# Kernel tuning notes

Hardware: AMD Instinct MI355X
Metric: run time of the kernel (lower is better)

The kernel has to match this reference:

```python
import jax, jax.numpy as jnp
import numpy as np

N = 20000
E = 400000
LATENT = 128
HIDDEN = 512
OUT = 64
HEADS = 4
NEG_SLOPE = 0.2


def setup_inputs() -> dict:
    key = jax.random.key(0)
    ks = jax.random.split(key, 12)
    z = jax.random.normal(ks[0], (N, LATENT), dtype=jnp.float32)
    edge_index = jax.random.randint(ks[1], (2, E), 0, N, dtype=jnp.int64)
    h1 = HIDDEN // 2
    # dense1, dense2 (torch Linear: y = x @ W.T + b; store W already transposed)
    W1 = jax.random.normal(ks[2], (LATENT, h1), dtype=jnp.float32) / np.sqrt(LATENT)
    b1 = jnp.zeros((h1,), dtype=jnp.float32)
    W2 = jax.random.normal(ks[3], (h1, HIDDEN), dtype=jnp.float32) / np.sqrt(h1)
    b2 = jnp.zeros((HIDDEN,), dtype=jnp.float32)
    # GATConv params
    Wg = jax.random.normal(ks[4], (HIDDEN, HEADS * OUT), dtype=jnp.float32) / np.sqrt(HIDDEN)
    att_src = jax.random.normal(ks[5], (HEADS, OUT), dtype=jnp.float32) * 0.1
    att_dst = jax.random.normal(ks[6], (HEADS, OUT), dtype=jnp.float32) * 0.1
    bias_g = jnp.zeros((OUT,), dtype=jnp.float32)
    return {"z": z, "W1": W1, "b1": b1, "W2": W2, "b2": b2,
            "Wg": Wg, "att_src": att_src, "att_dst": att_dst, "bias_g": bias_g,
            "edge_index": edge_index}


def _gat(x, Wg, att_src, att_dst, bias_g, src, dst):
    # project: [N, H, D]
    h = (x @ Wg).reshape(N, HEADS, OUT)
    a_src = jnp.einsum('nhd,hd->nh', h, att_src)  # [N, H]
    a_dst = jnp.einsum('nhd,hd->nh', h, att_dst)
    e = a_src[src] + a_dst[dst]                   # [E+N, H]
    e = jax.nn.leaky_relu(e, NEG_SLOPE)
    # segment softmax over destination nodes
    m = jax.ops.segment_max(e, dst, num_segments=N)
    e = jnp.exp(e - m[dst])
    denom = jax.ops.segment_sum(e, dst, num_segments=N)
    w = e / (denom[dst] + 1e-16)                  # [E+N, H]
    msg = h[src] * w[:, :, None]                  # [E+N, H, D]
    out = jax.ops.segment_sum(msg, dst, num_segments=N)  # [N, H, D]
    return out.mean(axis=1) + bias_g              # concat=False -> mean heads


def reference(z, W1, b1, W2, b2, Wg, att_src, att_dst, bias_g, edge_index):
    x = jax.nn.relu(z @ W1 + b1)
    x = jax.nn.relu(x @ W2 + b2)
    # PyG GATConv default add_self_loops=True
    loop = jnp.arange(N, dtype=edge_index.dtype)
    src = jnp.concatenate([edge_index[0], loop])
    dst = jnp.concatenate([edge_index[1], loop])
    return _gat(x, Wg, att_src, att_dst, bias_g, src, dst)
```

## Files before the change

### kernel.cpp

```cpp
#include <hip/hip_runtime.h>
#include <hip/hip_bf16.h>

#define N_NODES 20000
#define MPAD    20096
#define E_EDGES 400000
#define LATENT 128
#define H1 256
#define HIDDEN 512
#define OUT_D 64
#define HEADS 4
#define NEG_SLOPE 0.2f
#define MAX_IN 80

typedef __attribute__((ext_vector_type(8))) __bf16 bf16x8;
typedef __attribute__((ext_vector_type(4))) float f32x4;
typedef __attribute__((ext_vector_type(4))) unsigned short u16x4;
typedef __attribute__((ext_vector_type(8))) unsigned short u16x8;

__device__ __forceinline__ unsigned short f2bf(float f) {
    union { float f; unsigned int u; } v; v.f = f;
    unsigned int r = v.u + 0x7fffu + ((v.u >> 16) & 1u);
    return (unsigned short)(r >> 16);
}
__device__ __forceinline__ float bf2f(unsigned short u) {
    union { unsigned int u; float f; } v; v.u = ((unsigned int)u) << 16;
    return v.f;
}

#define W1_TILES 32
#define W2_TILES 128
#define WG_TILES 128
#define CUR_BLKS ((N_NODES + 255) / 256)
#define PREP_BLKS (W1_TILES + W2_TILES + WG_TILES + CUR_BLKS)
__global__ __launch_bounds__(256)
void prep_kernel(const float* __restrict__ W1, const float* __restrict__ W2,
                 const float* __restrict__ Wg,
                 unsigned short* __restrict__ W1t, unsigned short* __restrict__ W2t,
                 unsigned short* __restrict__ Wgt, int* __restrict__ cur) {
    int b = blockIdx.x;
    if (b >= W1_TILES + W2_TILES + WG_TILES) {
        int t = (b - (W1_TILES + W2_TILES + WG_TILES)) * 256 + threadIdx.x;
        if (t < N_NODES) cur[t] = 0;
        return;
    }
    const float* src; unsigned short* dst; int K, N, k0, n0;
    if (b < W1_TILES) {
        src = W1; dst = W1t; K = LATENT; N = H1;
        k0 = (b >> 3) * 32; n0 = (b & 7) * 32;
    } else if (b < W1_TILES + W2_TILES) {
        int t2 = b - W1_TILES;
        src = W2; dst = W2t; K = H1; N = HIDDEN;
        k0 = (t2 >> 4) * 32; n0 = (t2 & 15) * 32;
    } else {
        int t3 = b - W1_TILES - W2_TILES;
        src = Wg; dst = Wgt; K = HIDDEN; N = HEADS * OUT_D;
        k0 = (t3 >> 3) * 32; n0 = (t3 & 7) * 32;
    }
    __shared__ float tile[32][33];
    const int c = threadIdx.x & 31, r0 = threadIdx.x >> 5;
#pragma unroll
    for (int i = 0; i < 4; i++) {
        int r = r0 + i * 8;
        tile[r][c] = src[(size_t)(k0 + r) * N + n0 + c];
    }
    __syncthreads();
#pragma unroll
    for (int i = 0; i < 4; i++) {
        int r = r0 + i * 8;
        dst[(size_t)(n0 + r) * K + k0 + c] = f2bf(tile[c][r]);
    }
}

#define TM 32
#define ZPITCH 136
#define XPITCH 264
#define X2PITCH 520
#define MLP_BLOCKS (MPAD / TM)
#define SCAT_BLOCKS ((E_EDGES + 255) / 256)
__global__ __launch_bounds__(256, 4)
void mlp_scatter_kernel(const float* __restrict__ z,
                        const unsigned short* __restrict__ W1t,
                        const unsigned short* __restrict__ W2t,
                        const unsigned short* __restrict__ Wgt,
                        const float* __restrict__ b1, const float* __restrict__ b2,
                        const float* __restrict__ att_src, const float* __restrict__ att_dst,
                        const int* __restrict__ ei, int* __restrict__ cur,
                        int* __restrict__ adj,
                        unsigned short* __restrict__ hb,
                        float* __restrict__ a_src, float* __restrict__ a_dst) {
    __shared__ unsigned short x2s[TM * X2PITCH];
    __shared__ unsigned short x1s[TM * XPITCH];

    if (blockIdx.x >= MLP_BLOCKS) {
        int t = (blockIdx.x - MLP_BLOCKS) * 256 + threadIdx.x;
        if (t < E_EDGES) {
            int s = ei[t], d = ei[E_EDGES + t];
            int idx = atomicAdd(&cur[d], 1);
            idx = min(idx, MAX_IN - 1);
            adj[d * MAX_IN + idx] = s;
        }
        return;
    }

    unsigned short* zbf = x2s;
    const int tid = threadIdx.x;
    const int wave = tid >> 6, lane = tid & 63;
    const int m0 = blockIdx.x * TM;
    const int fr = lane & 15, q = lane >> 4;

#define LDW1(kt, t)      (*(const bf16x8*)(W1t + (size_t)(nb1 + (t) * 16 + fr) * LATENT + (kt) * 32 + q * 8))
#define LDW2H(nh, kt, t) (*(const bf16x8*)(W2t + (size_t)(nb2 + (nh) * 64 + (t) * 16 + fr) * H1 + (kt) * 32 + q * 8))
#define LDW3(kt, t)      (*(const bf16x8*)(Wgt + (size_t)(nb3 + (t) * 16 + fr) * HIDDEN + (kt) * 32 + q * 8))

    const int nb1 = wave * 64;
    const int nb2 = wave * 128;
    const int head = wave;
    const int nb3 = wave * 64;

    bf16x8 w1a[4], w1b[4];
#pragma unroll
    for (int t = 0; t < 4; t++) w1a[t] = LDW1(0, t);

    {
        const int r = tid >> 3, c0 = (tid & 7) * 16;
        const int zrow = min(m0 + r, N_NODES - 1);
        const float* zp = z + (size_t)zrow * LATENT + c0;
#pragma unroll
        for (int i = 0; i < 4; i++) {
            f32x4 v = *(const f32x4*)(zp + i * 4);
            u16x4 p = { f2bf(v[0]), f2bf(v[1]), f2bf(v[2]), f2bf(v[3]) };
            *(u16x4*)(zbf + r * ZPITCH + c0 + i * 4) = p;
        }
    }
    __syncthreads();

    f32x4 acc1[2][4] = {};
#pragma unroll
    for (int kt = 0; kt < 4; kt++) {
        bf16x8* wc = (kt & 1) ? w1b : w1a;
        bf16x8* wn = (kt & 1) ? w1a : w1b;
        if (kt < 3) {
#pragma unroll
            for (int t = 0; t < 4; t++) wn[t] = LDW1(kt + 1, t);
        }
        bf16x8 af[2];
#pragma unroll
        for (int t = 0; t < 2; t++)
            af[t] = *(const bf16x8*)(zbf + (t * 16 + fr) * ZPITCH + kt * 32 + q * 8);
#pragma unroll
        for (int mt = 0; mt < 2; mt++)
#pragma unroll
            for (int nt = 0; nt < 4; nt++)
                acc1[mt][nt] = __builtin_amdgcn_mfma_f32_16x16x32_bf16(
                    wc[nt], af[mt], acc1[mt][nt], 0, 0, 0);
    }

    bf16x8 w2a[4], w2b[4];
#pragma unroll
    for (int t = 0; t < 4; t++) w2a[t] = LDW2H(0, 0, t);

#pragma unroll
    for (int nt = 0; nt < 4; nt++) {
        const int n = nb1 + nt * 16 + q * 4;
        const f32x4 bv = *(const f32x4*)(b1 + n);
#pragma unroll
        for (int mt = 0; mt < 2; mt++) {
            u16x4 p;
#pragma unroll
            for (int r = 0; r < 4; r++) p[r] = f2bf(fmaxf(acc1[mt][nt][r] + bv[r], 0.f));
            *(u16x4*)(x1s + (mt * 16 + fr) * XPITCH + n) = p;
        }
    }
    __syncthreads();

#pragma unroll
    for (int nh = 0; nh < 2; nh++) {
        if (nh == 1) {
#pragma unroll
            for (int t = 0; t < 4; t++) w2a[t] = LDW2H(1, 0, t);
        }
        f32x4 acc2[2][4] = {};
#pragma unroll
        for (int kt = 0; kt < 8; kt++) {
            bf16x8* wc = (kt & 1) ? w2b : w2a;
            bf16x8* wn = (kt & 1) ? w2a : w2b;
            if (kt < 7) {
#pragma unroll
                for (int t = 0; t < 4; t++) wn[t] = LDW2H(nh, kt + 1, t);
            }
            bf16x8 af[2];
#pragma unroll
            for (int t = 0; t < 2; t++)
                af[t] = *(const bf16x8*)(x1s + (t * 16 + fr) * XPITCH + kt * 32 + q * 8);
#pragma unroll
            for (int mt = 0; mt < 2; mt++)
#pragma unroll
                for (int nt = 0; nt < 4; nt++)
                    acc2[mt][nt] = __builtin_amdgcn_mfma_f32_16x16x32_bf16(
                        wc[nt], af[mt], acc2[mt][nt], 0, 0, 0);
        }
#pragma unroll
        for (int nt = 0; nt < 4; nt++) {
            const int n = nb2 + nh * 64 + nt * 16 + q * 4;
            const f32x4 bv = *(const f32x4*)(b2 + n);
#pragma unroll
            for (int mt = 0; mt < 2; mt++) {
                u16x4 p;
#pragma unroll
                for (int r = 0; r < 4; r++) p[r] = f2bf(fmaxf(acc2[mt][nt][r] + bv[r], 0.f));
                *(u16x4*)(x2s + (mt * 16 + fr) * X2PITCH + n) = p;
            }
        }
    }

    bf16x8 w3a[4], w3b[4];
#pragma unroll
    for (int t = 0; t < 4; t++) w3a[t] = LDW3(0, t);
    __syncthreads();

    f32x4 acc3[2][4] = {};
#pragma unroll
    for (int kt = 0; kt < 16; kt++) {
        bf16x8* wc = (kt & 1) ? w3b : w3a;
        bf16x8* wn = (kt & 1) ? w3a : w3b;
        if (kt < 15) {
#pragma unroll
            for (int t = 0; t < 4; t++) wn[t] = LDW3(kt + 1, t);
        }
        bf16x8 af[2];
#pragma unroll
        for (int t = 0; t < 2; t++)
            af[t] = *(const bf16x8*)(x2s + (t * 16 + fr) * X2PITCH + kt * 32 + q * 8);
#pragma unroll
        for (int mt = 0; mt < 2; mt++)
#pragma unroll
            for (int nt = 0; nt < 4; nt++)
                acc3[mt][nt] = __builtin_amdgcn_mfma_f32_16x16x32_bf16(
                    wc[nt], af[mt], acc3[mt][nt], 0, 0, 0);
    }

    {
        f32x4 asv[4], adv[4];
#pragma unroll
        for (int nt = 0; nt < 4; nt++) {
            asv[nt] = *(const f32x4*)(att_src + head * OUT_D + nt * 16 + q * 4);
            adv[nt] = *(const f32x4*)(att_dst + head * OUT_D + nt * 16 + q * 4);
        }
#pragma unroll
        for (int mt = 0; mt < 2; mt++) {
            const int row = m0 + mt * 16 + fr;
            float vs = 0.f, vd = 0.f;
#pragma unroll
            for (int nt = 0; nt < 4; nt++) {
                u16x4 p;
#pragma unroll
                for (int r = 0; r < 4; r++) {
                    float x = acc3[mt][nt][r];
                    p[r] = f2bf(x);
                    vs += x * asv[nt][r];
                    vd += x * adv[nt][r];
                }
                *(u16x4*)(hb + (size_t)row * (HEADS * OUT_D) + head * OUT_D + nt * 16 + q * 4) = p;
            }
            vs += __shfl_xor(vs, 16, 64); vs += __shfl_xor(vs, 32, 64);
            vd += __shfl_xor(vd, 16, 64); vd += __shfl_xor(vd, 32, 64);
            if (q == 0 && row < N_NODES) {
                a_src[row * HEADS + head] = vs;
                a_dst[row * HEADS + head] = vd;
            }
        }
    }
#undef LDW1
#undef LDW2H
#undef LDW3
}

__global__ __launch_bounds__(256)
void fused_gat(const int* __restrict__ adj, const int* __restrict__ cur,
               const float* __restrict__ a_src, const float* __restrict__ a_dst,
               const unsigned short* __restrict__ hb,
               const float* __restrict__ bias_g, float* __restrict__ out) {
    const int wave = threadIdx.x >> 6, lane = threadIdx.x & 63;
    const int grp = lane >> 5, sl = lane & 31;
    const int d = blockIdx.x * 8 + wave * 2 + grp;
    const int h = sl >> 3, j = sl & 7;
    const int cnt = min(cur[d], MAX_IN);
    const int* arow = adj + d * MAX_IN;
    const int gbase = grp * 32;

    int myadj = (sl < cnt) ? arow[sl] : 0;

    const float ad = a_dst[d * HEADS + h];
    const unsigned short* hp = hb + h * OUT_D + j * 8;

    float vself = a_src[d * HEADS + h] + ad;
    vself = (vself > 0.f) ? vself : NEG_SLOPE * vself;
    float sm = __expf(fminf(vself, 60.f));
    u16x8 gs = *(const u16x8*)(hp + (size_t)d * (HEADS * OUT_D));
    float acc[8];
#pragma unroll
    for (int r = 0; r < 8; r++) acc[r] = sm * bf2f(gs[r]);

    const int lim = cnt < 32 ? cnt : 32;
    int e = 0;
    for (; e + 7 < lim; e += 8) {
        int sx[8]; float fx[8]; u16x8 gx[8];
#pragma unroll
        for (int u = 0; u < 8; u++) sx[u] = __shfl(myadj, gbase + e + u, 64);
#pragma unroll
        for (int u = 0; u < 8; u++) fx[u] = a_src[sx[u] * HEADS + h];
#pragma unroll
        for (int u = 0; u < 8; u++) gx[u] = *(const u16x8*)(hp + (size_t)sx[u] * (HEADS * OUT_D));
#pragma unroll
        for (int u = 0; u < 8; u++) {
            float v = fx[u] + ad;
            v = (v > 0.f) ? v : NEG_SLOPE * v;
            float w = __expf(fminf(v, 60.f));
            sm += w;
#pragma unroll
            for (int r = 0; r < 8; r++) acc[r] += w * bf2f(gx[u][r]);
        }
    }
    for (; e + 3 < lim; e += 4) {
        int sx[4]; float fx[4]; u16x8 gx[4];
#pragma unroll
        for (int u = 0; u < 4; u++) sx[u] = __shfl(myadj, gbase + e + u, 64);
#pragma unroll
        for (int u = 0; u < 4; u++) fx[u] = a_src[sx[u] * HEADS + h];
#pragma unroll
        for (int u = 0; u < 4; u++) gx[u] = *(const u16x8*)(hp + (size_t)sx[u] * (HEADS * OUT_D));
#pragma unroll
        for (int u = 0; u < 4; u++) {
            float v = fx[u] + ad;
            v = (v > 0.f) ? v : NEG_SLOPE * v;
            float w = __expf(fminf(v, 60.f));
            sm += w;
#pragma unroll
            for (int r = 0; r < 8; r++) acc[r] += w * bf2f(gx[u][r]);
        }
    }
    for (; e < lim; e++) {
        int s = __shfl(myadj, gbase + e, 64);
        float v = a_src[s * HEADS + h] + ad;
        v = (v > 0.f) ? v : NEG_SLOPE * v;
        float w = __expf(fminf(v, 60.f));
        u16x8 g = *(const u16x8*)(hp + (size_t)s * (HEADS * OUT_D));
        sm += w;
#pragma unroll
        for (int r = 0; r < 8; r++) acc[r] += w * bf2f(g[r]);
    }
    for (int e2 = 32; e2 < cnt; e2++) {
        int s = arow[e2];
        float v = a_src[s * HEADS + h] + ad;
        v = (v > 0.f) ? v : NEG_SLOPE * v;
        float w = __expf(fminf(v, 60.f));
        u16x8 g = *(const u16x8*)(hp + (size_t)s * (HEADS * OUT_D));
        sm += w;
#pragma unroll
        for (int r = 0; r < 8; r++) acc[r] += w * bf2f(g[r]);
    }

    const float inv = 1.f / (sm + 1e-16f);
#pragma unroll
    for (int r = 0; r < 8; r++) {
        acc[r] *= inv;
        acc[r] += __shfl_xor(acc[r], 8, 64);
        acc[r] += __shfl_xor(acc[r], 16, 64);
    }
    if (h == 0) {
        const f32x4 bg0 = *(const f32x4*)(bias_g + j * 8);
        const f32x4 bg1 = *(const f32x4*)(bias_g + j * 8 + 4);
        f32x4 o0 = { 0.25f * acc[0] + bg0[0], 0.25f * acc[1] + bg0[1],
                     0.25f * acc[2] + bg0[2], 0.25f * acc[3] + bg0[3] };
        f32x4 o1 = { 0.25f * acc[4] + bg1[0], 0.25f * acc[5] + bg1[1],
                     0.25f * acc[6] + bg1[2], 0.25f * acc[7] + bg1[3] };
        *(f32x4*)(out + (size_t)d * OUT_D + j * 8) = o0;
        *(f32x4*)(out + (size_t)d * OUT_D + j * 8 + 4) = o1;
    }
}

extern "C" void kernel_launch(void* const* d_in, const int* in_sizes, int n_in,
                              void* d_out, int out_size, void* d_ws, size_t ws_size,
                              hipStream_t stream) {
    const float* z       = (const float*)d_in[0];
    const float* W1      = (const float*)d_in[1];
    const float* b1      = (const float*)d_in[2];
    const float* W2      = (const float*)d_in[3];
    const float* b2      = (const float*)d_in[4];
    const float* Wg      = (const float*)d_in[5];
    const float* att_src = (const float*)d_in[6];
    const float* att_dst = (const float*)d_in[7];
    const float* bias_g  = (const float*)d_in[8];
    const int*   ei      = (const int*)d_in[9];
    float* out = (float*)d_out;

    char* ws = (char*)d_ws;
    size_t off = 0;
    auto carve = [&](size_t bytes) { void* p = ws + off; off += (bytes + 255) & ~(size_t)255; return p; };

    unsigned short* W1t = (unsigned short*)carve((size_t)H1 * LATENT * 2);
    unsigned short* W2t = (unsigned short*)carve((size_t)HIDDEN * H1 * 2);
    unsigned short* Wgt = (unsigned short*)carve((size_t)(HEADS * OUT_D) * HIDDEN * 2);
    unsigned short* hb  = (unsigned short*)carve((size_t)MPAD * HEADS * OUT_D * 2);
    float* a_src = (float*)carve((size_t)N_NODES * HEADS * 4);
    float* a_dst = (float*)carve((size_t)N_NODES * HEADS * 4);
    int*   cur   = (int*)carve((size_t)N_NODES * 4);
    int*   adj   = (int*)carve((size_t)MAX_IN * N_NODES * 4);

    prep_kernel<<<PREP_BLKS, 256, 0, stream>>>(W1, W2, Wg, W1t, W2t, Wgt, cur);

    mlp_scatter_kernel<<<MLP_BLOCKS + SCAT_BLOCKS, 256, 0, stream>>>(
        z, W1t, W2t, Wgt, b1, b2, att_src, att_dst, ei, cur, adj, hb, a_src, a_dst);

    fused_gat<<<N_NODES / 8, 256, 0, stream>>>(
        adj, cur, a_src, a_dst, hb, bias_g, out);
}
```

Before: 161.8 us.

## Merge MLP, edge scatter and GAT aggregation into one persistent kernel with grid barrier

Replaces the separate MLP/scatter and GAT aggregation launches with a single persistent kernel. Each block first scatters a strided share of edges into the adjacency lists, then runs its MLP tile. All blocks then meet at an atomic-counter grid barrier and finish with grid-stride GAT aggregation. The aim is to remove a kernel launch and its drain/fill gap. The cost is a spin barrier that depends on all 628 blocks being resident at once, which occupancy is hinted at 3 blocks per CU to allow, and fewer blocks in the gather phase.

Result: slower. 528.1 us (+226.4%).

```diff
diff --git a/kernel.cpp b/kernel.cpp
--- a/kernel.cpp
+++ b/kernel.cpp
@@ -36,11 +36,13 @@
 void prep_kernel(const float* __restrict__ W1, const float* __restrict__ W2,
                  const float* __restrict__ Wg,
                  unsigned short* __restrict__ W1t, unsigned short* __restrict__ W2t,
-                 unsigned short* __restrict__ Wgt, int* __restrict__ cur) {
+                 unsigned short* __restrict__ Wgt, int* __restrict__ cur,
+                 int* __restrict__ bar) {
     int b = blockIdx.x;
     if (b >= W1_TILES + W2_TILES + WG_TILES) {
         int t = (b - (W1_TILES + W2_TILES + WG_TILES)) * 256 + threadIdx.x;
         if (t < N_NODES) cur[t] = 0;
+        if (t == N_NODES) *bar = 0;
         return;
     }
     const float* src; unsigned short* dst; int K, N, k0, n0;
@@ -75,307 +77,318 @@
 #define ZPITCH 136
 #define XPITCH 264
 #define X2PITCH 520
-#define MLP_BLOCKS (MPAD / TM)
-#define SCAT_BLOCKS ((E_EDGES + 255) / 256)
-__global__ __launch_bounds__(256, 4)
-void mlp_scatter_kernel(const float* __restrict__ z,
-                        const unsigned short* __restrict__ W1t,
-                        const unsigned short* __restrict__ W2t,
-                        const unsigned short* __restrict__ Wgt,
-                        const float* __restrict__ b1, const float* __restrict__ b2,
-                        const float* __restrict__ att_src, const float* __restrict__ att_dst,
-                        const int* __restrict__ ei, int* __restrict__ cur,
-                        int* __restrict__ adj,
-                        unsigned short* __restrict__ hb,
-                        float* __restrict__ a_src, float* __restrict__ a_dst) {
+#define NBLOCKS (MPAD / TM)
+
+__global__ __launch_bounds__(256, 3)
+void mega2(const float* __restrict__ z,
+           const unsigned short* __restrict__ W1t,
+           const unsigned short* __restrict__ W2t,
+           const unsigned short* __restrict__ Wgt,
+           const float* __restrict__ b1, const float* __restrict__ b2,
+           const float* __restrict__ att_src, const float* __restrict__ att_dst,
+           const float* __restrict__ bias_g, const int* __restrict__ ei,
+           unsigned short* __restrict__ hb,
+           float* __restrict__ a_src, float* __restrict__ a_dst,
+           int* __restrict__ cur, int* __restrict__ adj,
+           int* __restrict__ bar, float* __restrict__ out) {
     __shared__ unsigned short x2s[TM * X2PITCH];
     __shared__ unsigned short x1s[TM * XPITCH];
 
-    if (blockIdx.x >= MLP_BLOCKS) {
-        int t = (blockIdx.x - MLP_BLOCKS) * 256 + threadIdx.x;
-        if (t < E_EDGES) {
+    {
+        int gid = blockIdx.x * 256 + threadIdx.x;
+        for (int t = gid; t < E_EDGES; t += NBLOCKS * 256) {
             int s = ei[t], d = ei[E_EDGES + t];
             int idx = atomicAdd(&cur[d], 1);
             idx = min(idx, MAX_IN - 1);
             adj[d * MAX_IN + idx] = s;
         }
-        return;
-    }
-
-    unsigned short* zbf = x2s;
-    const int tid = threadIdx.x;
-    const int wave = tid >> 6, lane = tid & 63;
-    const int m0 = blockIdx.x * TM;
-    const int fr = lane & 15, q = lane >> 4;
+    }
+
+    {
+        unsigned short* zbf = x2s;
+        const int tid = threadIdx.x;
+        const int wave = tid >> 6, lane = tid & 63;
+        const int m0 = blockIdx.x * TM;
+        const int fr = lane & 15, q = lane >> 4;
 
 #define LDW1(kt, t)      (*(const bf16x8*)(W1t + (size_t)(nb1 + (t) * 16 + fr) * LATENT + (kt) * 32 + q * 8))
 #define LDW2H(nh, kt, t) (*(const bf16x8*)(W2t + (size_t)(nb2 + (nh) * 64 + (t) * 16 + fr) * H1 + (kt) * 32 + q * 8))
 #define LDW3(kt, t)      (*(const bf16x8*)(Wgt + (size_t)(nb3 + (t) * 16 + fr) * HIDDEN + (kt) * 32 + q * 8))
 
-    const int nb1 = wave * 64;
-    const int nb2 = wave * 128;
-    const int head = wave;
-    const int nb3 = wave * 64;
-
-    bf16x8 w1a[4], w1b[4];
-#pragma unroll
-    for (int t = 0; t < 4; t++) w1a[t] = LDW1(0, t);
-
-    {
-        const int r = tid >> 3, c0 = (tid & 7) * 16;
-        const int zrow = min(m0 + r, N_NODES - 1);
-        const float* zp = z + (size_t)zrow * LATENT + c0;
-#pragma unroll
-        for (int i = 0; i < 4; i++) {
-            f32x4 v = *(const f32x4*)(zp + i * 4);
-            u16x4 p = { f2bf(v[0]), f2bf(v[1]), f2bf(v[2]), f2bf(v[3]) };
-            *(u16x4*)(zbf + r * ZPITCH + c0 + i * 4) = p;
-        }
-    }
-    __syncthreads();
-
-    f32x4 acc1[2][4] = {};
-#pragma unroll
-    for (int kt = 0; kt < 4; kt++) {
-        bf16x8* wc = (kt & 1) ? w1b : w1a;
-        bf16x8* wn = (kt & 1) ? w1a : w1b;
-        if (kt < 3) {
-#pragma unroll
-            for (int t = 0; t < 4; t++) wn[t] = LDW1(kt + 1, t);
-        }
-        bf16x8 af[2];
-#pragma unroll
-        for (int t = 0; t < 2; t++)
-            af[t] = *(const bf16x8*)(zbf + (t * 16 + fr) * ZPITCH + kt * 32 + q * 8);
-#pragma unroll
-        for (int mt = 0; mt < 2; mt++)
-#pragma unroll
-            for (int nt = 0; nt < 4; nt++)
-                acc1[mt][nt] = __builtin_amdgcn_mfma_f32_16x16x32_bf16(
-                    wc[nt], af[mt], acc1[mt][nt], 0, 0, 0);
-    }
-
-    bf16x8 w2a[4], w2b[4];
-#pragma unroll
-    for (int t = 0; t < 4; t++) w2a[t] = LDW2H(0, 0, t);
-
-#pragma unroll
-    for (int nt = 0; nt < 4; nt++) {
-        const int n = nb1 + nt * 16 + q * 4;
-        const f32x4 bv = *(const f32x4*)(b1 + n);
-#pragma unroll
-        for (int mt = 0; mt < 2; mt++) {
-            u16x4 p;
-#pragma unroll
-            for (int r = 0; r < 4; r++) p[r] = f2bf(fmaxf(acc1[mt][nt][r] + bv[r], 0.f));
-            *(u16x4*)(x1s + (mt * 16 + fr) * XPITCH + n) = p;
-        }
-    }
-    __syncthreads();
-
-#pragma unroll
-    for (int nh = 0; nh < 2; nh++) {
-        if (nh == 1) {
-#pragma unroll
-            for (int t = 0; t < 4; t++) w2a[t] = LDW2H(1, 0, t);
-        }
-        f32x4 acc2[2][4] = {};
-#pragma unroll
-        for (int kt = 0; kt < 8; kt++) {
-            bf16x8* wc = (kt & 1) ? w2b : w2a;
-            bf16x8* wn = (kt & 1) ? w2a : w2b;
-            if (kt < 7) {
-#pragma unroll
-                for (int t = 0; t < 4; t++) wn[t] = LDW2H(nh, kt + 1, t);
+        const int nb1 = wave * 64;
+        const int nb2 = wave * 128;
+        const int head = wave;
+        const int nb3 = wave * 64;
+
+        bf16x8 w1a[4], w1b[4];
+#pragma unroll
+        for (int t = 0; t < 4; t++) w1a[t] = LDW1(0, t);
+
+        {
+            const int r = tid >> 3, c0 = (tid & 7) * 16;
+            const int zrow = min(m0 + r, N_NODES - 1);
+            const float* zp = z + (size_t)zrow * LATENT + c0;
+#pragma unroll
+            for (int i = 0; i < 4; i++) {
+                f32x4 v = *(const f32x4*)(zp + i * 4);
+                u16x4 p = { f2bf(v[0]), f2bf(v[1]), f2bf(v[2]), f2bf(v[3]) };
+                *(u16x4*)(zbf + r * ZPITCH + c0 + i * 4) = p;
+            }
+        }
+        __syncthreads();
+
+        f32x4 acc1[2][4] = {};
+#pragma unroll
+        for (int kt = 0; kt < 4; kt++) {
+            bf16x8* wc = (kt & 1) ? w1b : w1a;
+            bf16x8* wn = (kt & 1) ? w1a : w1b;
+            if (kt < 3) {
+#pragma unroll
+                for (int t = 0; t < 4; t++) wn[t] = LDW1(kt + 1, t);
             }
             bf16x8 af[2];
 #pragma unroll
             for (int t = 0; t < 2; t++)
-                af[t] = *(const bf16x8*)(x1s + (t * 16 + fr) * XPITCH + kt * 32 + q * 8);
+                af[t] = *(const bf16x8*)(zbf + (t * 16 + fr) * ZPITCH + kt * 32 + q * 8);
 #pragma unroll
             for (int mt = 0; mt < 2; mt++)
 #pragma unroll
                 for (int nt = 0; nt < 4; nt++)
-                    acc2[mt][nt] = __builtin_amdgcn_mfma_f32_16x16x32_bf16(
-                        wc[nt], af[mt], acc2[mt][nt], 0, 0, 0);
-        }
+                    acc1[mt][nt] = __builtin_amdgcn_mfma_f32_16x16x32_bf16(
+                        wc[nt], af[mt], acc1[mt][nt], 0, 0, 0);
+        }
+
+        bf16x8 w2a[4], w2b[4];
+#pragma unroll
+        for (int t = 0; t < 4; t++) w2a[t] = LDW2H(0, 0, t);
+
 #pragma unroll
         for (int nt = 0; nt < 4; nt++) {
-            const int n = nb2 + nh * 64 + nt * 16 + q * 4;
-            const f32x4 bv = *(const f32x4*)(b2 + n);
+            const int n = nb1 + nt * 16 + q * 4;
+            const f32x4 bv = *(const f32x4*)(b1 + n);
 #pragma unroll
             for (int mt = 0; mt < 2; mt++) {
                 u16x4 p;
 #pragma unroll
-                for (int r = 0; r < 4; r++) p[r] = f2bf(fmaxf(acc2[mt][nt][r] + bv[r], 0.f));
-                *(u16x4*)(x2s + (mt * 16 + fr) * X2PITCH + n) = p;
-            }
-        }
-    }
-
-    bf16x8 w3a[4], w3b[4];
-#pragma unroll
-    for (int t = 0; t < 4; t++) w3a[t] = LDW3(0, t);
-    __syncthreads();
-
-    f32x4 acc3[2][4] = {};
-#pragma unroll
-    for (int kt = 0; kt < 16; kt++) {
-        bf16x8* wc = (kt & 1) ? w3b : w3a;
-        bf16x8* wn = (kt & 1) ? w3a : w3b;
-        if (kt < 15) {
-#pragma unroll
-            for (int t = 0; t < 4; t++) wn[t] = LDW3(kt + 1, t);
-        }
-        bf16x8 af[2];
-#pragma unroll
-        for (int t = 0; t < 2; t++)
-            af[t] = *(const bf16x8*)(x2s + (t * 16 + fr) * X2PITCH + kt * 32 + q * 8);
-#pragma unroll
-        for (int mt = 0; mt < 2; mt++)
-#pragma unroll
-            for (int nt = 0; nt < 4; nt++)
-                acc3[mt][nt] = __builtin_amdgcn_mfma_f32_16x16x32_bf16(
-                    wc[nt], af[mt], acc3[mt][nt], 0, 0, 0);
-    }
-
-    {
-        f32x4 asv[4], adv[4];
-#pragma unroll
-        for (int nt = 0; nt < 4; nt++) {
-            asv[nt] = *(const f32x4*)(att_src + head * OUT_D + nt * 16 + q * 4);
-            adv[nt] = *(const f32x4*)(att_dst + head * OUT_D + nt * 16 + q * 4);
-        }
-#pragma unroll
-        for (int mt = 0; mt < 2; mt++) {
-            const int row = m0 + mt * 16 + fr;
-            float vs = 0.f, vd = 0.f;
+                for (int r = 0; r < 4; r++) p[r] = f2bf(fmaxf(acc1[mt][nt][r] + bv[r], 0.f));
+                *(u16x4*)(x1s + (mt * 16 + fr) * XPITCH + n) = p;
+            }
+        }
+        __syncthreads();
+
+#pragma unroll
+        for (int nh = 0; nh < 2; nh++) {
+            if (nh == 1) {
+#pragma unroll
+                for (int t = 0; t < 4; t++) w2a[t] = LDW2H(1, 0, t);
+            }
+            f32x4 acc2[2][4] = {};
+#pragma unroll
+            for (int kt = 0; kt < 8; kt++) {
+                bf16x8* wc = (kt & 1) ? w2b : w2a;
+                bf16x8* wn = (kt & 1) ? w2a : w2b;
+                if (kt < 7) {
+#pragma unroll
+                    for (int t = 0; t < 4; t++) wn[t] = LDW2H(nh, kt + 1, t);
+                }
+                bf16x8 af[2];
+#pragma unroll
+                for (int t = 0; t < 2; t++)
+                    af[t] = *(const bf16x8*)(x1s + (t * 16 + fr) * XPITCH + kt * 32 + q * 8);
+#pragma unroll
+                for (int mt = 0; mt < 2; mt++)
+#pragma unroll
+                    for (int nt = 0; nt < 4; nt++)
+                        acc2[mt][nt] = __builtin_amdgcn_mfma_f32_16x16x32_bf16(
+                            wc[nt], af[mt], acc2[mt][nt], 0, 0, 0);
+            }
 #pragma unroll
             for (int nt = 0; nt < 4; nt++) {
-                u16x4 p;
-#pragma unroll
-                for (int r = 0; r < 4; r++) {
-                    float x = acc3[mt][nt][r];
-                    p[r] = f2bf(x);
-                    vs += x * asv[nt][r];
-                    vd += x * adv[nt][r];
-                }
-                *(u16x4*)(hb + (size_t)row * (HEADS * OUT_D) + head * OUT_D + nt * 16 + q * 4) = p;
-            }
-            vs += __shfl_xor(vs, 16, 64); vs += __shfl_xor(vs, 32, 64);
-            vd += __shfl_xor(vd, 16, 64); vd += __shfl_xor(vd, 32, 64);
-            if (q == 0 && row < N_NODES) {
-                a_src[row * HEADS + head] = vs;
-                a_dst[row * HEADS + head] = vd;
-            }
-        }
-    }
+                const int n = nb2 + nh * 64 + nt * 16 + q * 4;
+                const f32x4 bv = *(const f32x4*)(b2 + n);
+#pragma unroll
+                for (int mt = 0; mt < 2; mt++) {
+                    u16x4 p;
+#pragma unroll
+                    for (int r = 0; r < 4; r++) p[r] = f2bf(fmaxf(acc2[mt][nt][r] + bv[r], 0.f));
+                    *(u16x4*)(x2s + (mt * 16 + fr) * X2PITCH + n) = p;
+                }
+            }
+        }
+
+        bf16x8 w3a[4], w3b[4];
+#pragma unroll
+        for (int t = 0; t < 4; t++) w3a[t] = LDW3(0, t);
+        __syncthreads();
+
+        f32x4 acc3[2][4] = {};
+#pragma unroll
+        for (int kt = 0; kt < 16; kt++) {
+            bf16x8* wc = (kt & 1) ? w3b : w3a;
+            bf16x8* wn = (kt & 1) ? w3a : w3b;
+            if (kt < 15) {
+#pragma unroll
+                for (int t = 0; t < 4; t++) wn[t] = LDW3(kt + 1, t);
+            }
+            bf16x8 af[2];
+#pragma unroll
+            for (int t = 0; t < 2; t++)
+                af[t] = *(const bf16x8*)(x2s + (t * 16 + fr) * X2PITCH + kt * 32 + q * 8);
+#pragma unroll
+            for (int mt = 0; mt < 2; mt++)
+#pragma unroll
+                for (int nt = 0; nt < 4; nt++)
+                    acc3[mt][nt] = __builtin_amdgcn_mfma_f32_16x16x32_bf16(
+                        wc[nt], af[mt], acc3[mt][nt], 0, 0, 0);
+        }
+
+        {
+            f32x4 asv[4], adv[4];
+#pragma unroll
+            for (int nt = 0; nt < 4; nt++) {
+                asv[nt] = *(const f32x4*)(att_src + head * OUT_D + nt * 16 + q * 4);
+                adv[nt] = *(const f32x4*)(att_dst + head * OUT_D + nt * 16 + q * 4);
+            }
+#pragma unroll
+            for (int mt = 0; mt < 2; mt++) {
+                const int row = m0 + mt * 16 + fr;
+                float vs = 0.f, vd = 0.f;
+#pragma unroll
+                for (int nt = 0; nt < 4; nt++) {
+                    u16x4 p;
+#pragma unroll
+                    for (int r = 0; r < 4; r++) {
+                        float x = acc3[mt][nt][r];
+                        p[r] = f2bf(x);
+                        vs += x * asv[nt][r];
+                        vd += x * adv[nt][r];
+                    }
+                    *(u16x4*)(hb + (size_t)row * (HEADS * OUT_D) + head * OUT_D + nt * 16 + q * 4) = p;
+                }
+                vs += __shfl_xor(vs, 16, 64); vs += __shfl_xor(vs, 32, 64);
+                vd += __shfl_xor(vd, 16, 64); vd += __shfl_xor(vd, 32, 64);
+                if (q == 0 && row < N_NODES) {
+                    a_src[row * HEADS + head] = vs;
+                    a_dst[row * HEADS + head] = vd;
+                }
+            }
+        }
 #undef LDW1
 #undef LDW2H
 #undef LDW3
-}
-
-__global__ __launch_bounds__(256)
-void fused_gat(const int* __restrict__ adj, const int* __restrict__ cur,
-               const float* __restrict__ a_src, const float* __restrict__ a_dst,
-               const unsigned short* __restrict__ hb,
-               const float* __restrict__ bias_g, float* __restrict__ out) {
-    const int wave = threadIdx.x >> 6, lane = threadIdx.x & 63;
-    const int grp = lane >> 5, sl = lane & 31;
-    const int d = blockIdx.x * 8 + wave * 2 + grp;
-    const int h = sl >> 3, j = sl & 7;
-    const int cnt = min(cur[d], MAX_IN);
-    const int* arow = adj + d * MAX_IN;
-    const int gbase = grp * 32;
-
-    int myadj = (sl < cnt) ? arow[sl] : 0;
-
-    const float ad = a_dst[d * HEADS + h];
-    const unsigned short* hp = hb + h * OUT_D + j * 8;
-
-    float vself = a_src[d * HEADS + h] + ad;
-    vself = (vself > 0.f) ? vself : NEG_SLOPE * vself;
-    float sm = __expf(fminf(vself, 60.f));
-    u16x8 gs = *(const u16x8*)(hp + (size_t)d * (HEADS * OUT_D));
-    float acc[8];
-#pragma unroll
-    for (int r = 0; r < 8; r++) acc[r] = sm * bf2f(gs[r]);
-
-    const int lim = cnt < 32 ? cnt : 32;
-    int e = 0;
-    for (; e + 7 < lim; e += 8) {
-        int sx[8]; float fx[8]; u16x8 gx[8];
-#pragma unroll
-        for (int u = 0; u < 8; u++) sx[u] = __shfl(myadj, gbase + e + u, 64);
-#pragma unroll
-        for (int u = 0; u < 8; u++) fx[u] = a_src[sx[u] * HEADS + h];
-#pragma unroll
-        for (int u = 0; u < 8; u++) gx[u] = *(const u16x8*)(hp + (size_t)sx[u] * (HEADS * OUT_D));
-#pragma unroll
-        for (int u = 0; u < 8; u++) {
-            float v = fx[u] + ad;
-            v = (v > 0.f) ? v : NEG_SLOPE * v;
-            float w = __expf(fminf(v, 60.f));
-            sm += w;
-#pragma unroll
-            for (int r = 0; r < 8; r++) acc[r] += w * bf2f(gx[u][r]);
-        }
-    }
-    for (; e + 3 < lim; e += 4) {
-        int sx[4]; float fx[4]; u16x8 gx[4];
-#pragma unroll
-        for (int u = 0; u < 4; u++) sx[u] = __shfl(myadj, gbase + e + u, 64);
-#pragma unroll
-        for (int u = 0; u < 4; u++) fx[u] = a_src[sx[u] * HEADS + h];
-#pragma unroll
-        for (int u = 0; u < 4; u++) gx[u] = *(const u16x8*)(hp + (size_t)sx[u] * (HEADS * OUT_D));
-#pragma unroll
-        for (int u = 0; u < 4; u++) {
-            float v = fx[u] + ad;
-            v = (v > 0.f) ? v : NEG_SLOPE * v;
-            float w = __expf(fminf(v, 60.f));
-            sm += w;
-#pragma unroll
-            for (int r = 0; r < 8; r++) acc[r] += w * bf2f(gx[u][r]);
-        }
-    }
-    for (; e < lim; e++) {
-        int s = __shfl(myadj, gbase + e, 64);
-        float v = a_src[s * HEADS + h] + ad;
-        v = (v > 0.f) ? v : NEG_SLOPE * v;
-        float w = __expf(fminf(v, 60.f));
-        u16x8 g = *(const u16x8*)(hp + (size_t)s * (HEADS * OUT_D));
-        sm += w;
-#pragma unroll
-        for (int r = 0; r < 8; r++) acc[r] += w * bf2f(g[r]);
-    }
-    for (int e2 = 32; e2 < cnt; e2++) {
-        int s = arow[e2];
-        float v = a_src[s * HEADS + h] + ad;
-        v = (v > 0.f) ? v : NEG_SLOPE * v;
-        float w = __expf(fminf(v, 60.f));
-        u16x8 g = *(const u16x8*)(hp + (size_t)s * (HEADS * OUT_D));
-        sm += w;
-#pragma unroll
-        for (int r = 0; r < 8; r++) acc[r] += w * bf2f(g[r]);
-    }
-
-    const float inv = 1.f / (sm + 1e-16f);
-#pragma unroll
-    for (int r = 0; r < 8; r++) {
-        acc[r] *= inv;
-        acc[r] += __shfl_xor(acc[r], 8, 64);
-        acc[r] += __shfl_xor(acc[r], 16, 64);
-    }
-    if (h == 0) {
-        const f32x4 bg0 = *(const f32x4*)(bias_g + j * 8);
-        const f32x4 bg1 = *(const f32x4*)(bias_g + j * 8 + 4);
-        f32x4 o0 = { 0.25f * acc[0] + bg0[0], 0.25f * acc[1] + bg0[1],
-                     0.25f * acc[2] + bg0[2], 0.25f * acc[3] + bg0[3] };
-        f32x4 o1 = { 0.25f * acc[4] + bg1[0], 0.25f * acc[5] + bg1[1],
-                     0.25f * acc[6] + bg1[2], 0.25f * acc[7] + bg1[3] };
-        *(f32x4*)(out + (size_t)d * OUT_D + j * 8) = o0;
-        *(f32x4*)(out + (size_t)d * OUT_D + j * 8 + 4) = o1;
+    }
+
+    __threadfence();
+    __syncthreads();
+    if (threadIdx.x == 0) {
+        __hip_atomic_fetch_add(bar, 1, __ATOMIC_ACQ_REL, __HIP_MEMORY_SCOPE_AGENT);
+        while (__hip_atomic_load(bar, __ATOMIC_ACQUIRE, __HIP_MEMORY_SCOPE_AGENT) < NBLOCKS)
+            __builtin_amdgcn_s_sleep(2);
+    }
+    __syncthreads();
+    __threadfence();
+
+    {
+        const int wv = threadIdx.x >> 6, ln = threadIdx.x & 63;
+        const int grp = ln >> 5, sl = ln & 31;
+        const int h = sl >> 3, j = sl & 7;
+        const int gbase = grp * 32;
+
+        for (int d0 = blockIdx.x * 8; d0 < N_NODES; d0 += NBLOCKS * 8) {
+            const int d = d0 + wv * 2 + grp;
+            const int cnt = min(cur[d], MAX_IN);
+            const int* arow = adj + d * MAX_IN;
+
+            int myadj = (sl < cnt) ? arow[sl] : 0;
+
+            const float ad = a_dst[d * HEADS + h];
+            const unsigned short* hp = hb + h * OUT_D + j * 8;
+
+            float vself = a_src[d * HEADS + h] + ad;
+            vself = (vself > 0.f) ? vself : NEG_SLOPE * vself;
+            float sm = __expf(fminf(vself, 60.f));
+            u16x8 gs = *(const u16x8*)(hp + (size_t)d * (HEADS * OUT_D));
+            float acc[8];
+#pragma unroll
+            for (int r = 0; r < 8; r++) acc[r] = sm * bf2f(gs[r]);
+
+            const int lim = cnt < 32 ? cnt : 32;
+            int e = 0;
+            for (; e + 7 < lim; e += 8) {
+                int sx[8]; float fx[8]; u16x8 gx[8];
+#pragma unroll
+                for (int u = 0; u < 8; u++) sx[u] = __shfl(myadj, gbase + e + u, 64);
+#pragma unroll
+                for (int u = 0; u < 8; u++) fx[u] = a_src[sx[u] * HEADS + h];
+#pragma unroll
+                for (int u = 0; u < 8; u++) gx[u] = *(const u16x8*)(hp + (size_t)sx[u] * (HEADS * OUT_D));
+#pragma unroll
+                for (int u = 0; u < 8; u++) {
+                    float v = fx[u] + ad;
+                    v = (v > 0.f) ? v : NEG_SLOPE * v;
+                    float w = __expf(fminf(v, 60.f));
+                    sm += w;
+#pragma unroll
+                    for (int r = 0; r < 8; r++) acc[r] += w * bf2f(gx[u][r]);
+                }
+            }
+            for (; e + 3 < lim; e += 4) {
+                int sx[4]; float fx[4]; u16x8 gx[4];
+#pragma unroll
+                for (int u = 0; u < 4; u++) sx[u] = __shfl(myadj, gbase + e + u, 64);
+#pragma unroll
+                for (int u = 0; u < 4; u++) fx[u] = a_src[sx[u] * HEADS + h];
+#pragma unroll
+                for (int u = 0; u < 4; u++) gx[u] = *(const u16x8*)(hp + (size_t)sx[u] * (HEADS * OUT_D));
+#pragma unroll
+                for (int u = 0; u < 4; u++) {
+                    float v = fx[u] + ad;
+                    v = (v > 0.f) ? v : NEG_SLOPE * v;
+                    float w = __expf(fminf(v, 60.f));
+                    sm += w;
+#pragma unroll
+                    for (int r = 0; r < 8; r++) acc[r] += w * bf2f(gx[u][r]);
+                }
+            }
+            for (; e < lim; e++) {
+                int s = __shfl(myadj, gbase + e, 64);
+                float v = a_src[s * HEADS + h] + ad;
+                v = (v > 0.f) ? v : NEG_SLOPE * v;
+                float w = __expf(fminf(v, 60.f));
+                u16x8 g = *(const u16x8*)(hp + (size_t)s * (HEADS * OUT_D));
+                sm += w;
+#pragma unroll
+                for (int r = 0; r < 8; r++) acc[r] += w * bf2f(g[r]);
+            }
+            for (int e2 = 32; e2 < cnt; e2++) {
+                int s = arow[e2];
+                float v = a_src[s * HEADS + h] + ad;
+                v = (v > 0.f) ? v : NEG_SLOPE * v;
+                float w = __expf(fminf(v, 60.f));
+                u16x8 g = *(const u16x8*)(hp + (size_t)s * (HEADS * OUT_D));
+                sm += w;
+#pragma unroll
+                for (int r = 0; r < 8; r++) acc[r] += w * bf2f(g[r]);
+            }
+
+            const float inv = 1.f / (sm + 1e-16f);
+#pragma unroll
+            for (int r = 0; r < 8; r++) {
+                acc[r] *= inv;
+                acc[r] += __shfl_xor(acc[r], 8, 64);
+                acc[r] += __shfl_xor(acc[r], 16, 64);
+            }
+            if (h == 0) {
+                const f32x4 bg0 = *(const f32x4*)(bias_g + j * 8);
+                const f32x4 bg1 = *(const f32x4*)(bias_g + j * 8 + 4);
+                f32x4 o0 = { 0.25f * acc[0] + bg0[0], 0.25f * acc[1] + bg0[1],
+                             0.25f * acc[2] + bg0[2], 0.25f * acc[3] + bg0[3] };
+                f32x4 o1 = { 0.25f * acc[4] + bg1[0], 0.25f * acc[5] + bg1[1],
+                             0.25f * acc[6] + bg1[2], 0.25f * acc[7] + bg1[3] };
+                *(f32x4*)(out + (size_t)d * OUT_D + j * 8) = o0;
+                *(f32x4*)(out + (size_t)d * OUT_D + j * 8 + 4) = o1;
+            }
+        }
     }
 }
 
@@ -406,12 +419,11 @@
     float* a_dst = (float*)carve((size_t)N_NODES * HEADS * 4);
     int*   cur   = (int*)carve((size_t)N_NODES * 4);
     int*   adj   = (int*)carve((size_t)MAX_IN * N_NODES * 4);
-
-    prep_kernel<<<PREP_BLKS, 256, 0, stream>>>(W1, W2, Wg, W1t, W2t, Wgt, cur);
-
-    mlp_scatter_kernel<<<MLP_BLOCKS + SCAT_BLOCKS, 256, 0, stream>>>(
-        z, W1t, W2t, Wgt, b1, b2, att_src, att_dst, ei, cur, adj, hb, a_src, a_dst);
-
-    fused_gat<<<N_NODES / 8, 256, 0, stream>>>(
-        adj, cur, a_src, a_dst, hb, bias_g, out);
+    int*   bar   = (int*)carve(256);
+
+    prep_kernel<<<PREP_BLKS, 256, 0, stream>>>(W1, W2, Wg, W1t, W2t, Wgt, cur, bar);
+
+    mega2<<<NBLOCKS, 256, 0, stream>>>(
+        z, W1t, W2t, Wgt, b1, b2, att_src, att_dst, bias_g, ei,
+        hb, a_src, a_dst, cur, adj, bar, out);
 }
```
